# Performance work log

Hardware: AMD Instinct MI355X
Metric: run time of the kernel (lower is better)

## Reference

```python
import jax, jax.numpy as jnp
import numpy as np

L, B, S, D, H = 3, 2, 2048, 512, 8
HD = D // H
EPS = 1e-5
NEG = -1e9

def setup_inputs() -> dict:
    key = jax.random.key(0)
    ks = jax.random.split(key, 12)
    sc = 1.0 / np.sqrt(D)
    w = lambda k, shape: (jax.random.normal(k, shape, jnp.float32) * sc)
    return {
        'x': jax.random.normal(ks[0], (B, S, D), jnp.float32),
        'mask': jax.random.randint(ks[1], (B, S), 0, 2).astype(jnp.int32),
        'Wp': w(ks[2], (L, D, D)), 'bp': jnp.zeros((L, D), jnp.float32),
        'gamma': jnp.ones((L, D), jnp.float32), 'beta_ln': jnp.zeros((L, D), jnp.float32),
        'Wq': w(ks[3], (L, D, D)), 'bq': jnp.zeros((L, D), jnp.float32),
        'Wk': w(ks[4], (L, D, D)), 'bk': jnp.zeros((L, D), jnp.float32),
        'Wv': w(ks[5], (L, D, D)), 'bv': jnp.zeros((L, D), jnp.float32),
        'Wo': w(ks[6], (L, D, D)), 'bo': jnp.zeros((L, D), jnp.float32),
        'Wout': w(ks[7], (L * D, D)), 'bout': jnp.zeros((D,), jnp.float32),
    }

def reference(x, mask, Wp, bp, gamma, beta_ln, Wq, bq, Wk, bk, Wv, bv, Wo, bo, Wout, bout):
    # per-level input projection: [L,B,S,D]
    xl = jnp.einsum('bsd,lde->lbse', x, Wp) + bp[:, None, None, :]
    # LayerNorm over last dim
    m = xl.mean(-1, keepdims=True)
    v = xl.var(-1, keepdims=True)
    xn = (xl - m) / jnp.sqrt(v + EPS) * gamma[:, None, None, :] + beta_ln[:, None, None, :]
    proj = lambda W, b: (jnp.einsum('lbsd,lde->lbse', xn, W) + b[:, None, None, :]).reshape(L, B, S, H, HD)
    Q, K, V = proj(Wq, bq), proj(Wk, bk), proj(Wv, bv)
    scores = jnp.einsum('lbqhd,lbkhd->lbhqk', Q, K) / np.sqrt(HD).astype(np.float32)
    scores = jnp.where(mask[None, :, None, None, :] == 0, NEG, scores)
    attn = jax.nn.softmax(scores, axis=-1)  # dropout is identity in eval
    attended = jnp.einsum('lbhqk,lbkhd->lbqhd', attn, V).reshape(L, B, S, D)
    lev = jnp.einsum('lbsd,lde->lbse', attended, Wo) + bo[:, None, None, :]  # [L,B,S,D]
    combined = jnp.moveaxis(lev, 0, 2).reshape(B, S, L * D)  # concat levels on last dim
    return combined @ Wout + bout
```

## Files before the change

### kernel.cpp

```cpp
#include <hip/hip_runtime.h>

typedef unsigned short ushort_t;
typedef __attribute__((ext_vector_type(8))) short bf16x8;
typedef __attribute__((ext_vector_type(4))) float f32x4;
typedef __attribute__((ext_vector_type(4))) unsigned int u32x4;
typedef __attribute__((ext_vector_type(2))) unsigned int u32x2;

#define DI static __device__ __forceinline__

DI ushort_t f2bf(float f){
  unsigned u = __builtin_bit_cast(unsigned, f);
  u += 0x7fffu + ((u >> 16) & 1u);
  return (ushort_t)(u >> 16);
}
DI float bf2f(ushort_t h){ unsigned u = ((unsigned)h) << 16; return __builtin_bit_cast(float, u); }

DI unsigned cvt_pk_bf16(float a, float b){
  unsigned r;
  asm("v_cvt_pk_bf16_f32 %0, %1, %2" : "=v"(r) : "v"(a), "v"(b));
  return r;
}

DI float exp2_fast(float x){
  float r;
  asm("v_exp_f32 %0, %1" : "=v"(r) : "v"(x));
  return r;
}

DI void gload_lds16(const void* g, void* l){
  __builtin_amdgcn_global_load_lds((const __attribute__((address_space(1))) void*)g,
                                   (__attribute__((address_space(3))) void*)l, 16, 0, 0);
}

#define CLOG2E 0.18033688011112042f


DI void do_cast_seg(const float* __restrict__ in, ushort_t* __restrict__ out,
                    int i, int n4){
  if (i >= n4) return;
  float4 v = ((const float4*)in)[i];
  ushort_t r0 = f2bf(v.x), r1 = f2bf(v.y), r2 = f2bf(v.z), r3 = f2bf(v.w);
  ushort_t* o = out + (size_t)i * 4;
  o[0] = r0; o[1] = r1; o[2] = r2; o[3] = r3;
}

DI void do_transpose_seg(float* __restrict__ tile,
                         const float* __restrict__ src, ushort_t* __restrict__ dst,
                         int R, int C, int bx, int by, float scale, int tid){
  int c0 = bx * 32, r0 = by * 32;
  int tx = tid & 31, ty = tid >> 5;
  #pragma unroll
  for (int p = 0; p < 4; ++p)
    tile[(ty + p * 8) * 33 + tx] = src[(size_t)(r0 + ty + p * 8) * C + c0 + tx];
  __syncthreads();
  #pragma unroll
  for (int p = 0; p < 4; ++p){
    int rr = ty + p * 8;
    dst[(size_t)(c0 + rr) * R + r0 + tx] = f2bf(tile[tx * 33 + rr] * scale);
  }
}


__global__ __launch_bounds__(256)
void prep_kernel(const float* __restrict__ x, const float* __restrict__ Wo,
                 const float* __restrict__ Wp, const float* __restrict__ Wout,
                 ushort_t* __restrict__ xb, ushort_t* __restrict__ WoB,
                 ushort_t* __restrict__ WpT, ushort_t* __restrict__ WoutT,
                 float* __restrict__ zbias){
  __shared__ float tile[32 * 33];
  const int bid = blockIdx.x, tid = threadIdx.x;
  if (bid < 2048){
    do_cast_seg(x, xb, bid * 256 + tid, 524288);
  } else if (bid < 2816){
    do_cast_seg(Wo, WoB, (bid - 2048) * 256 + tid, 196608);
  } else if (bid < 3584){
    int r = bid - 2816;
    int zz = r >> 8, t = r & 255;
    do_transpose_seg(tile, Wp + zz * 262144, WpT + zz * 262144, 512, 512,
                     t & 15, t >> 4, 1.0f, tid);
  } else if (bid < 4352){
    int t = bid - 3584;
    do_transpose_seg(tile, Wout, WoutT, 1536, 512, t & 15, t >> 4, 1.0f, tid);
  } else {
    int i = (bid - 4352) * 256 + tid;
    if (i < 512) zbias[i] = 0.f;
  }
}


__global__ __launch_bounds__(256)
void compact_kernel(const ushort_t* __restrict__ VtD, const int* __restrict__ pos,
                    ushort_t* __restrict__ KC, ushort_t* __restrict__ VtC){
  const int zb = blockIdx.y, b = zb & 1;
  const int tid = threadIdx.x;
  const int xb_ = blockIdx.x;
  if (xb_ < 128){
    const int g = xb_;
    const int nl = pos[b * 2049 + 2048];
    const int nt2e = ((((nl + 63) >> 6) + 1) & ~1) * 64;
    int pp[9];
    #pragma unroll
    for (int j = 0; j < 9; ++j) pp[j] = pos[b * 2049 + tid * 8 + j];
    const size_t rbase = (size_t)zb * 512 + g * 4;
    #pragma unroll
    for (int rr = 0; rr < 4; ++rr){
      const ushort_t* src = VtD + (rbase + rr) * 2048 + tid * 8;
      ushort_t* dstrow = VtC + (rbase + rr) * 2048;
      bf16x8 v = *(const bf16x8*)src;
      #pragma unroll
      for (int j = 0; j < 8; ++j)
        if (pp[j + 1] > pp[j]) dstrow[pp[j]] = (ushort_t)v[j];
      for (int ccol = nl + tid; ccol < nt2e; ccol += 256) dstrow[ccol] = 0;
    }
  } else {
    const int nl = pos[b * 2049 + 2048];
    const int nt2e = ((((nl + 63) >> 6) + 1) & ~1) * 64;
    const int padShorts = (nt2e - nl) * 512;
    bf16x8 zz = {};
    for (int j = tid * 8; j < padShorts; j += 2048)
      *(bf16x8*)(KC + ((size_t)zb * 2048 + nl) * 512 + j) = zz;
  }
}


template<int BN>
DI void gemm_mainloop(ushort_t* __restrict__ smem,
                      const ushort_t* __restrict__ A, const ushort_t* __restrict__ Bt,
                      int K, int lda, int ldb, int n0, int m0,
                      f32x4 (&acc)[4][BN / 32]){
  constexpr int NB = BN / 32;
  ushort_t* const As0 = smem;
  ushort_t* const Bs0 = smem + 2 * 128 * 32;
  const int tid = threadIdx.x, wid = tid >> 6, lane = tid & 63;
  const int wr = wid >> 1, wc = wid & 1, lr = lane & 15, lk = lane >> 4;

  auto stage = [&](int buf, int k0){
    ushort_t* const Ad = As0 + buf * (128 * 32);
    ushort_t* const Bd = Bs0 + buf * (BN * 32);
    #pragma unroll
    for (int i = 0; i < 2; ++i){
      const int ch = i * 256 + tid;
      const int row = ch >> 2, cc = ch & 3;
      gload_lds16(A + (size_t)(m0 + row) * lda + (k0 + cc * 8),
                  Ad + (i * 256 + wid * 64) * 8);
    }
    if (BN == 64){
      const int ch = tid;
      const int row = ch >> 2, cc = ch & 3;
      gload_lds16(Bt + (size_t)(n0 + row) * ldb + (k0 + cc * 8),
                  Bd + (wid * 64) * 8);
    } else {
      const int ch = (wid & 1) * 64 + lane;
      const int row = ch >> 2, cc = ch & 3;
      gload_lds16(Bt + (size_t)(n0 + row) * ldb + (k0 + cc * 8),
                  Bd + ((wid & 1) * 64) * 8);
    }
  };

  stage(0, 0);
  __syncthreads();

  const int nk = K >> 5;
  for (int t = 0; t < nk; ++t){
    const int cur = t & 1;
    if (t + 1 < nk) stage(cur ^ 1, (t + 1) * 32);

    const ushort_t* const Ac = As0 + cur * (128 * 32);
    const ushort_t* const Bc = Bs0 + cur * (BN * 32);
    bf16x8 af[4], bfr[NB];
    #pragma unroll
    for (int m = 0; m < 4; ++m)
      af[m] = *(const bf16x8*)&Ac[(wr * 64 + m * 16 + lr) * 32 + lk * 8];
    #pragma unroll
    for (int n = 0; n < NB; ++n)
      bfr[n] = *(const bf16x8*)&Bc[(wc * (BN / 2) + n * 16 + lr) * 32 + lk * 8];
    #pragma unroll
    for (int m = 0; m < 4; ++m)
      #pragma unroll
      for (int n = 0; n < NB; ++n)
        acc[m][n] = __builtin_amdgcn_mfma_f32_16x16x32_bf16(af[m], bfr[n], acc[m][n], 0, 0, 0);

    __syncthreads();
  }
}

template<int BF16OUT, int BN>
DI void gemm_store(const f32x4 (&acc)[4][BN / 32], const float* __restrict__ bias,
                   void* __restrict__ Cv, int n0, int m0, int ldc){
  constexpr int NB = BN / 32;
  const int tid = threadIdx.x, wid = tid >> 6, lane = tid & 63;
  const int wr = wid >> 1, wc = wid & 1, lr = lane & 15, lk = lane >> 4;
  #pragma unroll
  for (int n = 0; n < NB; ++n){
    const int col = n0 + wc * (BN / 2) + n * 16 + lr;
    const float bv = bias[col];
    #pragma unroll
    for (int m = 0; m < 4; ++m){
      const int row0 = m0 + wr * 64 + m * 16 + lk * 4;
      #pragma unroll
      for (int j = 0; j < 4; ++j){
        const float v = acc[m][n][j] + bv;
        const size_t idx = (size_t)(row0 + j) * ldc + col;
        if (BF16OUT) ((ushort_t*)Cv)[idx] = f2bf(v);
        else         ((float*)Cv)[idx] = v;
      }
    }
  }
}


template<int BF16OUT, int BN, int VT>
__global__ __launch_bounds__(256)
void gemm_bt(const ushort_t* __restrict__ A, const ushort_t* __restrict__ Bt,
             const float* __restrict__ bias, void* __restrict__ Cv,
             int M, int N, int K, int lda, int ldb, int ldc,
             long long sA, long long sB, long long sC, long long sBias,
             ushort_t* __restrict__ VtD, ushort_t* __restrict__ KCp,
             const int* __restrict__ pos){
  constexpr int NB = BN / 32;
  __shared__ ushort_t smem[2 * (128 + BN) * 32];
  const int gx = gridDim.x, gy = gridDim.y;
  const int nwg = gx * gy * gridDim.z;
  int flat = blockIdx.x + gx * (blockIdx.y + gy * blockIdx.z);
  flat = (flat & 7) * (nwg >> 3) + (flat >> 3);
  const int bxi = flat % gx;
  const int byi = (flat / gx) % gy;
  const int z   = flat / (gx * gy);

  A += (size_t)z * sA; Bt += (size_t)z * sB; bias += (size_t)z * sBias;
  const int n0 = bxi * BN, m0 = byi * 128;
  const int tid = threadIdx.x, wid = tid >> 6, lane = tid & 63;
  const int wr = wid >> 1, wc = wid & 1, lr = lane & 15, lk = lane >> 4;

  f32x4 acc[4][NB] = {};
  gemm_mainloop<BN>(smem, A, Bt, K, lda, ldb, n0, m0, acc);

  if (VT && n0 >= 1024){
    #pragma unroll
    for (int n = 0; n < NB; ++n){
      const int c = wc * (BN / 2) + n * 16 + lr;
      const float bv = bias[n0 + c];
      #pragma unroll
      for (int m = 0; m < 4; ++m){
        const int r0 = wr * 64 + m * 16 + lk * 4;
        u32x2 pk;
        pk[0] = cvt_pk_bf16(acc[m][n][0] + bv, acc[m][n][1] + bv);
        pk[1] = cvt_pk_bf16(acc[m][n][2] + bv, acc[m][n][3] + bv);
        *(u32x2*)&smem[c * 128 + (r0 ^ ((c & 7) << 3))] = pk;
      }
    }
    __syncthreads();
    constexpr int TPC = 256 / BN;
    constexpr int SPT = 128 / TPC;
    const int d_ = tid / TPC, sq = tid % TPC;
    const int gcol = n0 + d_;
    const int hh = (gcol - 1024) >> 6, dd = gcol & 63;
    const int b_ = m0 >> 11, s0g = m0 & 2047;
    ushort_t* dst = VtD + (((size_t)(z * 2 + b_) * 8 + hh) * 64 + dd) * 2048 + s0g;
    #pragma unroll
    for (int it = 0; it < SPT / 8; ++it){
      const int s0 = sq * SPT + it * 8;
      bf16x8 v = *(const bf16x8*)&smem[d_ * 128 + (s0 ^ ((d_ & 7) << 3))];
      *(bf16x8*)&dst[s0] = v;
    }
    return;
  }

  if (VT && n0 >= 512){
    #pragma unroll
    for (int n = 0; n < NB; ++n){
      const int c = wc * (BN / 2) + n * 16 + lr;
      const float bv = bias[n0 + c];
      #pragma unroll
      for (int m = 0; m < 4; ++m){
        const int r0 = wr * 64 + m * 16 + lk * 4;
        #pragma unroll
        for (int j = 0; j < 4; ++j)
          smem[(r0 + j) * 64 + c] = f2bf(acc[m][n][j] + bv);
      }
    }
    __syncthreads();
    const int b_ = m0 >> 11;
    const int sbase = m0 & 2047;
    const int* posb = pos + b_ * 2049;
    ushort_t* const KCz = KCp + (size_t)(z * 2 + b_) * 2048 * 512;
    const int col0 = n0 - 512;
    #pragma unroll
    for (int it = 0; it < 4; ++it){
      const int idx = it * 256 + tid;
      const int r = idx >> 3, cc8 = idx & 7;
      const int p0 = posb[sbase + r], p1 = posb[sbase + r + 1];
      if (p1 > p0){
        const bf16x8 v = *(const bf16x8*)&smem[r * 64 + cc8 * 8];
        *(bf16x8*)&KCz[(size_t)p0 * 512 + col0 + cc8 * 8] = v;
      }
    }
    return;
  }

  void* Cz = BF16OUT ? (void*)((ushort_t*)Cv + (size_t)z * sC)
                     : (void*)((float*)Cv + (size_t)z * sC);
  gemm_store<BF16OUT, BN>(acc, bias, Cz, n0, m0, ldc);
}


__global__ __launch_bounds__(256)
void gemm_dual(const ushort_t* __restrict__ WoutT, const ushort_t* __restrict__ WoB,
               const float* __restrict__ zbias, ushort_t* __restrict__ WcombT,
               const ushort_t* __restrict__ xb, const ushort_t* __restrict__ WpT,
               const float* __restrict__ bp, ushort_t* __restrict__ xlb,
               const float* __restrict__ Wq, const float* __restrict__ Wk,
               const float* __restrict__ Wv, ushort_t* __restrict__ WqkvT,
               const float* __restrict__ bq, const float* __restrict__ bk,
               const float* __restrict__ bv, float* __restrict__ bqkv,
               const int* __restrict__ mask, ushort_t* __restrict__ monesC,
               int* __restrict__ pos,
               const float* __restrict__ bo, const float* __restrict__ Wout,
               const float* __restrict__ bout, float* __restrict__ bcomb){
  __shared__ ushort_t smem[2 * (128 + 64) * 32];
  __shared__ int lds_scan[4];
  __shared__ int lds_nl;
  const int bid = blockIdx.x, tid = threadIdx.x;

  if (bid < 864){
    f32x4 acc[4][2] = {};
    if (bid < 96){
      const int bx = bid & 7, by = (bid >> 3) & 3, z = bid >> 5;
      gemm_mainloop<64>(smem, WoutT + z * 512, WoB + (size_t)z * 262144,
                        512, 1536, 512, bx * 64, by * 128, acc);
      gemm_store<1, 64>(acc, zbias, WcombT + (size_t)z * 512, bx * 64, by * 128, 1536);
    } else {
      int b2 = bid - 96;
      b2 = (b2 & 7) * 96 + (b2 >> 3);
      const int bx = b2 % 24, by = b2 / 24;
      gemm_mainloop<64>(smem, xb, WpT, 512, 512, 512, bx * 64, by * 128, acc);
      gemm_store<1, 64>(acc, bp, xlb, bx * 64, by * 128, 1536);
    }
  } else if (bid < 3168){
    float* tile = (float*)smem;
    int idx = bid - 864;
    int w = idx / 768, r = idx % 768;
    int zz = r >> 8, t = r & 255;
    int bx = t & 15, by = t >> 4;
    if (w == 0)      do_transpose_seg(tile, Wq + zz * 262144, WqkvT + (size_t)zz * 786432, 512, 512, bx, by, CLOG2E, tid);
    else if (w == 1) do_transpose_seg(tile, Wk + zz * 262144, WqkvT + 262144 + (size_t)zz * 786432, 512, 512, bx, by, 1.0f, tid);
    else             do_transpose_seg(tile, Wv + zz * 262144, WqkvT + 524288 + (size_t)zz * 786432, 512, 512, bx, by, 1.0f, tid);
  } else if (bid < 3186){
    int i = (bid - 3168) * 256 + tid;
    if (i < 4608){
      int l = i / 1536, j = i % 1536;
      float v = (j < 512) ? bq[l * 512 + j] * CLOG2E
              : (j < 1024 ? bk[l * 512 + j - 512] : bv[l * 512 + j - 1024]);
      bqkv[i] = v;
    }
  } else if (bid < 3188){
    const int b = bid - 3186;
    int v[8]; int s8 = 0;
    #pragma unroll
    for (int i = 0; i < 8; ++i){ v[i] = mask[b * 2048 + tid * 8 + i] ? 1 : 0; s8 += v[i]; }
    const int lane = tid & 63, wid2 = tid >> 6;
    int ws = s8;
    #pragma unroll
    for (int off = 1; off < 64; off <<= 1){
      int t = __shfl_up(ws, off);
      if (lane >= off) ws += t;
    }
    if (lane == 63) lds_scan[wid2] = ws;
    __syncthreads();
    int woff = 0;
    for (int w = 0; w < wid2; ++w) woff += lds_scan[w];
    int run = woff + ws - s8;
    #pragma unroll
    for (int i = 0; i < 8; ++i){ pos[b * 2049 + tid * 8 + i] = run; run += v[i]; }
    if (tid == 255){ pos[b * 2049 + 2048] = run; lds_nl = run; }
    __syncthreads();
    const int nl = lds_nl;
    #pragma unroll
    for (int i = 0; i < 8; ++i){
      int j = tid * 8 + i;
      monesC[b * 2048 + j] = (j < nl) ? (ushort_t)0x3F80 : (ushort_t)0;
    }
  } else {
    int wid = tid >> 6, lane = tid & 63;
    int n = (bid - 3188) * 4 + wid;
    float s = 0.f;
    #pragma unroll
    for (int it = 0; it < 24; ++it){
      int k = it * 64 + lane;
      s += bo[k] * Wout[(size_t)k * 512 + n];
    }
    #pragma unroll
    for (int off = 32; off; off >>= 1) s += __shfl_xor(s, off);
    if (lane == 0) bcomb[n] = s + bout[n];
  }
}


__global__ __launch_bounds__(256)
void ln_kernel(const ushort_t* __restrict__ xlb, ushort_t* __restrict__ xn,
               const float* __restrict__ gamma, const float* __restrict__ beta){
  int rid = blockIdx.x * 4 + (threadIdx.x >> 6);
  int lane = threadIdx.x & 63;
  int l = rid >> 12, bs = rid & 4095;
  const ushort_t* row = xlb + (size_t)bs * 1536 + l * 512;
  ushort_t* orow = xn + (size_t)bs * 1536 + l * 512;
  const bf16x8 a = *(const bf16x8*)(row + lane * 8);
  float vals[8];
  #pragma unroll
  for (int j = 0; j < 8; ++j) vals[j] = bf2f((ushort_t)a[j]);
  float s = 0.f, ss = 0.f;
  #pragma unroll
  for (int j = 0; j < 8; ++j){ s += vals[j]; ss += vals[j] * vals[j]; }
  #pragma unroll
  for (int off = 32; off; off >>= 1){
    s += __shfl_xor(s, off);
    ss += __shfl_xor(ss, off);
  }
  float mean = s * (1.0f / 512.0f);
  float var = ss * (1.0f / 512.0f) - mean * mean;
  float inv = rsqrtf(var + 1e-5f);
  const float* g = gamma + l * 512 + lane * 8;
  const float* be = beta + l * 512 + lane * 8;
  float4 g0 = ((const float4*)g)[0], g1 = ((const float4*)g)[1];
  float4 be0 = ((const float4*)be)[0], be1 = ((const float4*)be)[1];
  float gs[8] = {g0.x, g0.y, g0.z, g0.w, g1.x, g1.y, g1.z, g1.w};
  float bs8[8] = {be0.x, be0.y, be0.z, be0.w, be1.x, be1.y, be1.z, be1.w};
  bf16x8 r;
  #pragma unroll
  for (int j = 0; j < 8; ++j)
    r[j] = (short)f2bf((vals[j] - mean) * inv * gs[j] + bs8[j]);
  *(bf16x8*)(orow + lane * 8) = r;
}


__global__ __launch_bounds__(256)
void attn_kernel(const ushort_t* __restrict__ QbD, const ushort_t* __restrict__ KC,
                 const ushort_t* __restrict__ VtC, const ushort_t* __restrict__ mones,
                 const int* __restrict__ pos, ushort_t* __restrict__ att){
  const int hz = blockIdx.x, qb = blockIdx.y;
  const int h = hz & 7, z = hz >> 3;
  const int l = z >> 1, b = z & 1;
  const ushort_t* Qb = QbD + ((size_t)l * 4096 + b * 2048) * 512 + h * 64;
  const ushort_t* Kb = KC + (size_t)z * 2048 * 512 + h * 64;
  const ushort_t* Vt = VtC + ((size_t)(z * 8 + h) * 64) * 2048;

  const int nl = pos[b * 2049 + 2048];
  const int nt2 = (((nl + 63) >> 6) + 1) & ~1;

  __shared__ __attribute__((aligned(16))) ushort_t Ks[2][64 * 64];
  __shared__ __attribute__((aligned(16))) ushort_t Vs[2][64 * 64];

  const int tid = threadIdx.x, wid = tid >> 6, lane = tid & 63;
  const int lr = lane & 15, lk = lane >> 4;
  const int sw = lr & 7;
  const int qrow = qb * 64 + wid * 16 + lr;

  const ushort_t* qp = Qb + (size_t)qrow * 512 + lk * 8;
  const bf16x8 q0 = *(const bf16x8*)qp;
  const bf16x8 q1 = *(const bf16x8*)(qp + 32);

  const int ch0 = wid * 64 + lane, ch1 = 256 + wid * 64 + lane;
  const int r0_ = ch0 >> 3, c0_ = (ch0 & 7) ^ (r0_ & 7);
  const int r1_ = ch1 >> 3, c1_ = (ch1 & 7) ^ (r1_ & 7);
  const ushort_t* kg0 = Kb + (size_t)r0_ * 512 + c0_ * 8;
  const ushort_t* kg1 = Kb + (size_t)r1_ * 512 + c1_ * 8;
  const ushort_t* vg0 = Vt + (size_t)r0_ * 2048 + c0_ * 8;
  const ushort_t* vg1 = Vt + (size_t)r1_ * 2048 + c1_ * 8;
  ushort_t* const kdA0 = &Ks[0][(wid * 64) * 8];
  ushort_t* const kdA1 = &Ks[0][(256 + wid * 64) * 8];
  ushort_t* const kdB0 = &Ks[1][(wid * 64) * 8];
  ushort_t* const kdB1 = &Ks[1][(256 + wid * 64) * 8];
  ushort_t* const vdA0 = &Vs[0][(wid * 64) * 8];
  ushort_t* const vdA1 = &Vs[0][(256 + wid * 64) * 8];
  ushort_t* const vdB0 = &Vs[1][(wid * 64) * 8];
  ushort_t* const vdB1 = &Vs[1][(256 + wid * 64) * 8];

  const ushort_t* const kbA0 = &Ks[0][lr * 64 + (lk ^ sw) * 8];
  const ushort_t* const kbA4 = &Ks[0][lr * 64 + ((lk ^ sw) ^ 4) * 8];
  const ushort_t* const kbB0 = &Ks[1][lr * 64 + (lk ^ sw) * 8];
  const ushort_t* const kbB4 = &Ks[1][lr * 64 + ((lk ^ sw) ^ 4) * 8];
  const ushort_t* const vbA0 = &Vs[0][lr * 64 + (lk ^ sw) * 8];
  const ushort_t* const vbA4 = &Vs[0][lr * 64 + ((lk ^ sw) ^ 4) * 8];
  const ushort_t* const vbB0 = &Vs[1][lr * 64 + (lk ^ sw) * 8];
  const ushort_t* const vbB4 = &Vs[1][lr * 64 + ((lk ^ sw) ^ 4) * 8];

  const ushort_t* pm = mones + b * 2048 + lk * 8;

  f32x4 o[4] = {};
  f32x4 lrun = {0.f, 0.f, 0.f, 0.f};

  gload_lds16(kg0, kdA0); gload_lds16(kg1, kdA1);
  gload_lds16(vg0, vdA0); gload_lds16(vg1, vdA1);
  kg0 += 32768; kg1 += 32768; vg0 += 64; vg1 += 64;
  __syncthreads();

  auto tile_step = [&](const ushort_t* kb0, const ushort_t* kb4,
                       const ushort_t* vb0, const ushort_t* vb4,
                       ushort_t* sk0, ushort_t* sk1, ushort_t* sv0, ushort_t* sv1,
                       bool doStage){
    if (doStage){
      gload_lds16(kg0, sk0); gload_lds16(kg1, sk1);
      gload_lds16(vg0, sv0); gload_lds16(vg1, sv1);
      kg0 += 32768; kg1 += 32768; vg0 += 64; vg1 += 64;
    }
    const bf16x8 mo0 = *(const bf16x8*)pm;
    const bf16x8 mo1 = *(const bf16x8*)(pm + 32);
    pm += 64;

    f32x4 t[4];
    __builtin_amdgcn_s_setprio(1);
    #pragma unroll
    for (int hh = 0; hh < 4; ++hh){
      const bf16x8 kf0 = *(const bf16x8*)(kb0 + hh * 1024);
      const bf16x8 kf1 = *(const bf16x8*)(kb4 + hh * 1024);
      f32x4 tt = {0.f, 0.f, 0.f, 0.f};
      tt = __builtin_amdgcn_mfma_f32_16x16x32_bf16(kf0, q0, tt, 0, 0, 0);
      tt = __builtin_amdgcn_mfma_f32_16x16x32_bf16(kf1, q1, tt, 0, 0, 0);
      t[hh] = tt;
    }
    __builtin_amdgcn_s_setprio(0);

    unsigned a00, a01, a10, a11, a20, a21, a30, a31;
    a00 = cvt_pk_bf16(exp2_fast(t[0][0]), exp2_fast(t[0][1]));
    a01 = cvt_pk_bf16(exp2_fast(t[0][2]), exp2_fast(t[0][3]));
    a10 = cvt_pk_bf16(exp2_fast(t[1][0]), exp2_fast(t[1][1]));
    a11 = cvt_pk_bf16(exp2_fast(t[1][2]), exp2_fast(t[1][3]));
    a20 = cvt_pk_bf16(exp2_fast(t[2][0]), exp2_fast(t[2][1]));
    a21 = cvt_pk_bf16(exp2_fast(t[2][2]), exp2_fast(t[2][3]));
    a30 = cvt_pk_bf16(exp2_fast(t[3][0]), exp2_fast(t[3][1]));
    a31 = cvt_pk_bf16(exp2_fast(t[3][2]), exp2_fast(t[3][3]));
    asm("v_permlane32_swap_b32 %0, %1" : "+v"(a00), "+v"(a10));
    asm("v_permlane32_swap_b32 %0, %1" : "+v"(a01), "+v"(a11));
    asm("v_permlane32_swap_b32 %0, %1" : "+v"(a20), "+v"(a30));
    asm("v_permlane32_swap_b32 %0, %1" : "+v"(a21), "+v"(a31));
    asm("v_permlane16_swap_b32 %0, %1" : "+v"(a00), "+v"(a10));
    asm("v_permlane16_swap_b32 %0, %1" : "+v"(a01), "+v"(a11));
    asm("v_permlane16_swap_b32 %0, %1" : "+v"(a20), "+v"(a30));
    asm("v_permlane16_swap_b32 %0, %1" : "+v"(a21), "+v"(a31));
    const u32x4 f0 = {a00, a01, a10, a11};
    const u32x4 f1 = {a20, a21, a30, a31};
    const bf16x8 pf0 = __builtin_bit_cast(bf16x8, f0);
    const bf16x8 pf1 = __builtin_bit_cast(bf16x8, f1);

    __builtin_amdgcn_s_setprio(1);
    lrun = __builtin_amdgcn_mfma_f32_16x16x32_bf16(pf0, mo0, lrun, 0, 0, 0);
    lrun = __builtin_amdgcn_mfma_f32_16x16x32_bf16(pf1, mo1, lrun, 0, 0, 0);
    #pragma unroll
    for (int n = 0; n < 4; ++n){
      const bf16x8 v0 = *(const bf16x8*)(vb0 + n * 1024);
      const bf16x8 v1 = *(const bf16x8*)(vb4 + n * 1024);
      o[n] = __builtin_amdgcn_mfma_f32_16x16x32_bf16(pf0, v0, o[n], 0, 0, 0);
      o[n] = __builtin_amdgcn_mfma_f32_16x16x32_bf16(pf1, v1, o[n], 0, 0, 0);
    }
    __builtin_amdgcn_s_setprio(0);
    __syncthreads();
  };

  for (int kt2 = 0; kt2 < nt2; kt2 += 2){
    tile_step(kbA0, kbA4, vbA0, vbA4, kdB0, kdB1, vdB0, vdB1, true);
    tile_step(kbB0, kbB4, vbB0, vbB4, kdA0, kdA1, vdA0, vdA1, kt2 + 2 < nt2);
  }

  float invj[4];
  #pragma unroll
  for (int j = 0; j < 4; ++j) invj[j] = 1.0f / lrun[j];
  const size_t arow0 = (size_t)(b * 2048 + qb * 64 + wid * 16);
  #pragma unroll
  for (int n = 0; n < 4; ++n)
    #pragma unroll
    for (int j = 0; j < 4; ++j)
      att[(arow0 + lk * 4 + j) * 1536 + l * 512 + h * 64 + n * 16 + lr] = f2bf(o[n][j] * invj[j]);
}


extern "C" void kernel_launch(void* const* d_in, const int* in_sizes, int n_in,
                              void* d_out, int out_size, void* d_ws, size_t ws_size,
                              hipStream_t stream){
  const float* x    = (const float*)d_in[0];
  const int*   mask = (const int*)d_in[1];
  const float* Wp   = (const float*)d_in[2];
  const float* bp   = (const float*)d_in[3];
  const float* gamma= (const float*)d_in[4];
  const float* beta = (const float*)d_in[5];
  const float* Wq   = (const float*)d_in[6];
  const float* bq   = (const float*)d_in[7];
  const float* Wk   = (const float*)d_in[8];
  const float* bk   = (const float*)d_in[9];
  const float* Wv   = (const float*)d_in[10];
  const float* bv   = (const float*)d_in[11];
  const float* Wo   = (const float*)d_in[12];
  const float* bo   = (const float*)d_in[13];
  const float* Wout = (const float*)d_in[14];
  const float* bout = (const float*)d_in[15];

  char* ws = (char*)d_ws;
  size_t off = 0;
  auto alloc = [&](size_t bytes){ void* p = ws + off; off += (bytes + 255) & ~(size_t)255; return p; };
  ushort_t* xb    = (ushort_t*)alloc(4096ull * 512 * 2);
  ushort_t* WpT   = (ushort_t*)alloc(1536ull * 512 * 2);
  ushort_t* WqkvT = (ushort_t*)alloc(3ull * 1536 * 512 * 2);
  ushort_t* WoB   = (ushort_t*)alloc(3ull * 512 * 512 * 2);
  ushort_t* WoutT = (ushort_t*)alloc(512ull * 1536 * 2);
  ushort_t* WcombT= (ushort_t*)alloc(512ull * 1536 * 2);
  float*    bqkv  = (float*)alloc(3ull * 1536 * 4);
  float*    zbias = (float*)alloc(512ull * 4);
  float*    bcomb = (float*)alloc(512ull * 4);
  ushort_t* monesC= (ushort_t*)alloc(4096ull * 2);
  int*      pos   = (int*)alloc(2ull * 2049 * 4);
  char*     xlbuf = (char*)alloc(4096ull * 1536 * 4);
  ushort_t* xn    = (ushort_t*)alloc(4096ull * 1536 * 2);
  ushort_t* QbD   = (ushort_t*)alloc(3ull * 4096 * 512 * 2);
  ushort_t* VtD   = (ushort_t*)alloc(6ull * 512 * 2048 * 2);
  ushort_t* KC    = (ushort_t*)alloc(6ull * 2048 * 512 * 2);
  ushort_t* xlb   = (ushort_t*)xlbuf;
  ushort_t* att   = (ushort_t*)xlbuf;
  ushort_t* VtC   = (ushort_t*)(xlbuf + 12582912);

  prep_kernel<<<4354, 256, 0, stream>>>(x, Wo, Wp, Wout,
                                        xb, WoB, WpT, WoutT, zbias);

  gemm_dual<<<3316, 256, 0, stream>>>(WoutT, WoB, zbias, WcombT, xb, WpT, bp, xlb,
                                      Wq, Wk, Wv, WqkvT, bq, bk, bv, bqkv,
                                      mask, monesC, pos, bo, Wout, bout, bcomb);

  ln_kernel<<<3072, 256, 0, stream>>>(xlb, xn, gamma, beta);
  gemm_bt<1, 64, 1><<<dim3(24, 32, 3), 256, 0, stream>>>(xn, WqkvT, bqkv, QbD,
      4096, 1536, 512, 1536, 512, 512, 512, 786432, 4096ll * 512, 1536,
      VtD, KC, pos);
  compact_kernel<<<dim3(129, 6), 256, 0, stream>>>(VtD, pos, KC, VtC);
  attn_kernel<<<dim3(48, 32, 1), 256, 0, stream>>>(QbD, KC, VtC, monesC, pos, att);
  gemm_bt<0, 32, 0><<<dim3(16, 32, 1), 256, 0, stream>>>(att, WcombT, bcomb, (float*)d_out,
      4096, 512, 1536, 1536, 1536, 512, 0, 0, 0, 0, nullptr, nullptr, nullptr);
}
```

Measured before the change: 156.3 us.

## Fuse fp32-to-bf16 casts of x and Wo into GEMM mainloop operand loads

Drops the separate cast passes that turned x and Wo into bf16 workspace buffers in the prep kernel. A new GEMM mainloop variant loads the fp32 operand directly into registers, converts it with packed bf16 conversion, and writes it to LDS after the MFMAs, while the other operand still uses direct global-to-LDS loads. This removes a write and re-read of bf16 copies and shrinks the prep kernel. In exchange, the GEMM reads twice the bytes for that operand and converts it again in every tile that reuses it, and the register-staged path may hide latency less well than async LDS loads.

```diff
diff --git a/kernel.cpp b/kernel.cpp
--- a/kernel.cpp
+++ b/kernel.cpp
@@ -35,15 +35,6 @@
 #define CLOG2E 0.18033688011112042f
 
 
-DI void do_cast_seg(const float* __restrict__ in, ushort_t* __restrict__ out,
-                    int i, int n4){
-  if (i >= n4) return;
-  float4 v = ((const float4*)in)[i];
-  ushort_t r0 = f2bf(v.x), r1 = f2bf(v.y), r2 = f2bf(v.z), r3 = f2bf(v.w);
-  ushort_t* o = out + (size_t)i * 4;
-  o[0] = r0; o[1] = r1; o[2] = r2; o[3] = r3;
-}
-
 DI void do_transpose_seg(float* __restrict__ tile,
                          const float* __restrict__ src, ushort_t* __restrict__ dst,
                          int R, int C, int bx, int by, float scale, int tid){
@@ -62,27 +53,20 @@
 
 
 __global__ __launch_bounds__(256)
-void prep_kernel(const float* __restrict__ x, const float* __restrict__ Wo,
-                 const float* __restrict__ Wp, const float* __restrict__ Wout,
-                 ushort_t* __restrict__ xb, ushort_t* __restrict__ WoB,
+void prep_kernel(const float* __restrict__ Wp, const float* __restrict__ Wout,
                  ushort_t* __restrict__ WpT, ushort_t* __restrict__ WoutT,
                  float* __restrict__ zbias){
   __shared__ float tile[32 * 33];
   const int bid = blockIdx.x, tid = threadIdx.x;
-  if (bid < 2048){
-    do_cast_seg(x, xb, bid * 256 + tid, 524288);
-  } else if (bid < 2816){
-    do_cast_seg(Wo, WoB, (bid - 2048) * 256 + tid, 196608);
-  } else if (bid < 3584){
-    int r = bid - 2816;
-    int zz = r >> 8, t = r & 255;
+  if (bid < 768){
+    int zz = bid >> 8, t = bid & 255;
     do_transpose_seg(tile, Wp + zz * 262144, WpT + zz * 262144, 512, 512,
                      t & 15, t >> 4, 1.0f, tid);
-  } else if (bid < 4352){
-    int t = bid - 3584;
+  } else if (bid < 1536){
+    int t = bid - 768;
     do_transpose_seg(tile, Wout, WoutT, 1536, 512, t & 15, t >> 4, 1.0f, tid);
   } else {
-    int i = (bid - 4352) * 256 + tid;
+    int i = (bid - 1536) * 256 + tid;
     if (i < 512) zbias[i] = 0.f;
   }
 }
@@ -180,6 +164,89 @@
       for (int n = 0; n < NB; ++n)
         acc[m][n] = __builtin_amdgcn_mfma_f32_16x16x32_bf16(af[m], bfr[n], acc[m][n], 0, 0, 0);
 
+    __syncthreads();
+  }
+}
+
+
+template<int AF32>
+DI void gemm_mainloop_mx(ushort_t* __restrict__ smem,
+                         const void* __restrict__ Av, const void* __restrict__ Btv,
+                         int K, int lda, int ldb, int n0, int m0,
+                         f32x4 (&acc)[4][2]){
+  ushort_t* const As0 = smem;
+  ushort_t* const Bs0 = smem + 2 * 128 * 32;
+  const int tid = threadIdx.x, wid = tid >> 6, lane = tid & 63;
+  const int wr = wid >> 1, wc = wid & 1, lr = lane & 15, lk = lane >> 4;
+
+  u32x4 rk[2];
+
+  auto issue = [&](int buf, int k0){
+    if (AF32){
+      #pragma unroll
+      for (int i = 0; i < 2; ++i){
+        const int ch = i * 256 + tid;
+        const int row = ch >> 2, cc = ch & 3;
+        const float* src = (const float*)Av + (size_t)(m0 + row) * lda + k0 + cc * 8;
+        float4 a0 = *(const float4*)src, a1 = *(const float4*)(src + 4);
+        rk[i][0] = cvt_pk_bf16(a0.x, a0.y); rk[i][1] = cvt_pk_bf16(a0.z, a0.w);
+        rk[i][2] = cvt_pk_bf16(a1.x, a1.y); rk[i][3] = cvt_pk_bf16(a1.z, a1.w);
+      }
+      const int ch = tid;
+      const int row = ch >> 2, cc = ch & 3;
+      gload_lds16((const ushort_t*)Btv + (size_t)(n0 + row) * ldb + (k0 + cc * 8),
+                  Bs0 + buf * (64 * 32) + (wid * 64) * 8);
+    } else {
+      #pragma unroll
+      for (int i = 0; i < 2; ++i){
+        const int ch = i * 256 + tid;
+        const int row = ch >> 2, cc = ch & 3;
+        gload_lds16((const ushort_t*)Av + (size_t)(m0 + row) * lda + (k0 + cc * 8),
+                    As0 + buf * (128 * 32) + (i * 256 + wid * 64) * 8);
+      }
+      const int ch = tid;
+      const int row = ch >> 2, cc = ch & 3;
+      const float* src = (const float*)Btv + (size_t)(n0 + row) * ldb + k0 + cc * 8;
+      float4 a0 = *(const float4*)src, a1 = *(const float4*)(src + 4);
+      rk[0][0] = cvt_pk_bf16(a0.x, a0.y); rk[0][1] = cvt_pk_bf16(a0.z, a0.w);
+      rk[0][2] = cvt_pk_bf16(a1.x, a1.y); rk[0][3] = cvt_pk_bf16(a1.z, a1.w);
+    }
+  };
+  auto writeback = [&](int buf){
+    if (AF32){
+      #pragma unroll
+      for (int i = 0; i < 2; ++i)
+        *(u32x4*)&As0[buf * (128 * 32) + (i * 256 + tid) * 8] = rk[i];
+    } else {
+      *(u32x4*)&Bs0[buf * (64 * 32) + tid * 8] = rk[0];
+    }
+  };
+
+  issue(0, 0);
+  writeback(0);
+  __syncthreads();
+
+  const int nk = K >> 5;
+  for (int t = 0; t < nk; ++t){
+    const int cur = t & 1;
+    if (t + 1 < nk) issue(cur ^ 1, (t + 1) * 32);
+
+    const ushort_t* const Ac = As0 + cur * (128 * 32);
+    const ushort_t* const Bc = Bs0 + cur * (64 * 32);
+    bf16x8 af[4], bfr[2];
+    #pragma unroll
+    for (int m = 0; m < 4; ++m)
+      af[m] = *(const bf16x8*)&Ac[(wr * 64 + m * 16 + lr) * 32 + lk * 8];
+    #pragma unroll
+    for (int n = 0; n < 2; ++n)
+      bfr[n] = *(const bf16x8*)&Bc[(wc * 32 + n * 16 + lr) * 32 + lk * 8];
+    #pragma unroll
+    for (int m = 0; m < 4; ++m)
+      #pragma unroll
+      for (int n = 0; n < 2; ++n)
+        acc[m][n] = __builtin_amdgcn_mfma_f32_16x16x32_bf16(af[m], bfr[n], acc[m][n], 0, 0, 0);
+
+    if (t + 1 < nk) writeback(cur ^ 1);
     __syncthreads();
   }
 }
@@ -305,9 +372,9 @@
 
 
 __global__ __launch_bounds__(256)
-void gemm_dual(const ushort_t* __restrict__ WoutT, const ushort_t* __restrict__ WoB,
+void gemm_dual(const ushort_t* __restrict__ WoutT, const float* __restrict__ Wo,
                const float* __restrict__ zbias, ushort_t* __restrict__ WcombT,
-               const ushort_t* __restrict__ xb, const ushort_t* __restrict__ WpT,
+               const float* __restrict__ x, const ushort_t* __restrict__ WpT,
                const float* __restrict__ bp, ushort_t* __restrict__ xlb,
                const float* __restrict__ Wq, const float* __restrict__ Wk,
                const float* __restrict__ Wv, ushort_t* __restrict__ WqkvT,
@@ -326,14 +393,14 @@
     f32x4 acc[4][2] = {};
     if (bid < 96){
       const int bx = bid & 7, by = (bid >> 3) & 3, z = bid >> 5;
-      gemm_mainloop<64>(smem, WoutT + z * 512, WoB + (size_t)z * 262144,
-                        512, 1536, 512, bx * 64, by * 128, acc);
+      gemm_mainloop_mx<0>(smem, WoutT + z * 512, Wo + (size_t)z * 262144,
+                          512, 1536, 512, bx * 64, by * 128, acc);
       gemm_store<1, 64>(acc, zbias, WcombT + (size_t)z * 512, bx * 64, by * 128, 1536);
     } else {
       int b2 = bid - 96;
       b2 = (b2 & 7) * 96 + (b2 >> 3);
       const int bx = b2 % 24, by = b2 / 24;
-      gemm_mainloop<64>(smem, xb, WpT, 512, 512, 512, bx * 64, by * 128, acc);
+      gemm_mainloop_mx<1>(smem, x, WpT, 512, 512, 512, bx * 64, by * 128, acc);
       gemm_store<1, 64>(acc, bp, xlb, bx * 64, by * 128, 1536);
     }
   } else if (bid < 3168){
@@ -596,10 +663,8 @@
   char* ws = (char*)d_ws;
   size_t off = 0;
   auto alloc = [&](size_t bytes){ void* p = ws + off; off += (bytes + 255) & ~(size_t)255; return p; };
-  ushort_t* xb    = (ushort_t*)alloc(4096ull * 512 * 2);
   ushort_t* WpT   = (ushort_t*)alloc(1536ull * 512 * 2);
   ushort_t* WqkvT = (ushort_t*)alloc(3ull * 1536 * 512 * 2);
-  ushort_t* WoB   = (ushort_t*)alloc(3ull * 512 * 512 * 2);
   ushort_t* WoutT = (ushort_t*)alloc(512ull * 1536 * 2);
   ushort_t* WcombT= (ushort_t*)alloc(512ull * 1536 * 2);
   float*    bqkv  = (float*)alloc(3ull * 1536 * 4);
@@ -616,10 +681,9 @@
   ushort_t* att   = (ushort_t*)xlbuf;
   ushort_t* VtC   = (ushort_t*)(xlbuf + 12582912);
 
-  prep_kernel<<<4354, 256, 0, stream>>>(x, Wo, Wp, Wout,
-                                        xb, WoB, WpT, WoutT, zbias);
-
-  gemm_dual<<<3316, 256, 0, stream>>>(WoutT, WoB, zbias, WcombT, xb, WpT, bp, xlb,
+  prep_kernel<<<1538, 256, 0, stream>>>(Wp, Wout, WpT, WoutT, zbias);
+
+  gemm_dual<<<3316, 256, 0, stream>>>(WoutT, Wo, zbias, WcombT, x, WpT, bp, xlb,
                                       Wq, Wk, Wv, WqkvT, bq, bk, bv, bqkv,
                                       mask, monesC, pos, bo, Wout, bout, bcomb);
 
```

Result: slower. 161.7 us (+3.5%).
